# Optimization experiments

Hardware: AMD Instinct MI355X
Metric: run time of the kernel (lower is better)

Reference implementation:

```python
import jax, jax.numpy as jnp
import numpy as np

B, LI, LT = 1, 2048, 256
HID, HEADS, HD = 3072, 24, 128
MLP = 4 * HID  # 12288
EPS = 1e-6


def setup_inputs() -> dict:
    key = jax.random.key(0)
    ks = jax.random.split(key, 12)
    n = lambda k, s, sc=1.0: jax.random.normal(k, s, dtype=jnp.float32) * sc
    # RoPE tables, interleaved-pair layout over head_dim
    theta = 10000.0 ** (-jnp.arange(0, HD, 2, dtype=jnp.float32) / HD)  # [HD/2]
    ang = jnp.arange(LI, dtype=jnp.float32)[:, None] * theta[None, :]   # [LI, HD/2]
    freqs_cos = jnp.repeat(jnp.cos(ang), 2, axis=-1)  # [LI, HD]
    freqs_sin = jnp.repeat(jnp.sin(ang), 2, axis=-1)
    return {
        "img": n(ks[0], (B, LI, HID)),
        "txt": n(ks[1], (B, LT, HID)),
        "vec": n(ks[2], (B, HID)),
        "freqs_cos": freqs_cos,
        "freqs_sin": freqs_sin,
        "w1": n(ks[3], (3 * HID + MLP, HID), 0.02),
        "b1": jnp.zeros((3 * HID + MLP,), jnp.float32),
        "w2": n(ks[4], (HID, HID + MLP), 0.02),
        "b2": jnp.zeros((HID,), jnp.float32),
        "q_norm_w": jnp.ones((HD,), jnp.float32),
        "k_norm_w": jnp.ones((HD,), jnp.float32),
        "mod_w": n(ks[5], (3 * HID, HID), 0.02),
        "mod_b": jnp.zeros((3 * HID,), jnp.float32),
        "txt_len": LT,
    }


def _layernorm(x):  # no affine, eps=1e-6
    mu = x.mean(-1, keepdims=True)
    var = ((x - mu) ** 2).mean(-1, keepdims=True)
    return (x - mu) * jax.lax.rsqrt(var + EPS)


def _rmsnorm(x, w):  # per-head-dim RMSNorm with affine weight
    ms = (x * x).mean(-1, keepdims=True)
    return x * jax.lax.rsqrt(ms + EPS) * w


def _rope(x, cos, sin):  # x: [B,L,H,D]; interleaved complex rotation
    xr = x.reshape(*x.shape[:-1], HD // 2, 2)
    rot = jnp.stack([-xr[..., 1], xr[..., 0]], axis=-1).reshape(x.shape)
    return x * cos[None, :, None, :] + rot * sin[None, :, None, :]


def reference(img, txt, vec, freqs_cos, freqs_sin, w1, b1, w2, b2,
              q_norm_w, k_norm_w, mod_w, mod_b, txt_len):
    H = img.shape[-1]
    Li = img.shape[1]
    # modulation: SiLU(vec) @ W -> shift, scale, gate
    mod = jax.nn.silu(vec) @ mod_w.T + mod_b           # [B, 3H]
    shift, scale, gate = jnp.split(mod, 3, axis=-1)
    modulate = lambda x: x * (1.0 + scale[:, None, :]) + shift[:, None, :]
    img_mod = modulate(_layernorm(img))
    txt_mod = modulate(_layernorm(txt))
    x_mod = jnp.concatenate([img_mod, txt_mod], axis=1)  # [B,S,H]
    Bb, S = x_mod.shape[0], x_mod.shape[1]
    # fused QKV projection (slices of linear1)
    qkv = x_mod @ w1[: 3 * H].T + b1[: 3 * H]
    q, k, v = [t.reshape(Bb, S, HEADS, HD) for t in jnp.split(qkv, 3, axis=-1)]
    q = _rmsnorm(q, q_norm_w)
    k = _rmsnorm(k, k_norm_w)
    # RoPE only on the img portion of the sequence
    q = jnp.concatenate([_rope(q[:, :Li], freqs_cos, freqs_sin), q[:, Li:]], axis=1)
    k = jnp.concatenate([_rope(k[:, :Li], freqs_cos, freqs_sin), k[:, Li:]], axis=1)
    # full (non-causal) attention over img+txt tokens
    logits = jnp.einsum('bqhd,bkhd->bhqk', q, k) * (HD ** -0.5)
    probs = jax.nn.softmax(logits, axis=-1)
    attn = jnp.einsum('bhqk,bkhd->bqhd', probs, v).reshape(Bb, S, H)
    # MLP branch (linear1 mlp slice) with gelu-tanh, then fused linear2
    mlp = jax.nn.gelu(x_mod @ w1[3 * H:].T + b1[3 * H:], approximate=True)
    out = jnp.concatenate([attn, mlp], axis=-1) @ w2.T + b2  # [B,S,H]
    img_out = img + gate[:, None, :] * out[:, :-txt_len]
    txt_out = txt + gate[:, None, :] * out[:, -txt_len:]
    return img_out, txt_out
```

## Files before the change

### kernel.cpp

```cpp
#include <hip/hip_runtime.h>
#include <hip/hip_bf16.h>

#define DI __device__ __forceinline__

typedef __attribute__((ext_vector_type(8))) short bf8;
typedef __attribute__((ext_vector_type(4))) float f4;
typedef __attribute__((ext_vector_type(8))) unsigned short us8;

#define LI    2048
#define LT    256
#define SEQ   2304
#define HID   3072
#define NHEAD 24
#define HD    128
#define N1    21504
#define QKVW  9216
#define N2CAT 15360

DI unsigned short f2bf(float f) {
  union { float f; unsigned u; } v; v.f = f;
  unsigned r = v.u + 0x7FFFu + ((v.u >> 16) & 1u);
  return (unsigned short)(r >> 16);
}
DI float bf2f(unsigned short h) {
  union { unsigned u; float f; } v; v.u = ((unsigned)h) << 16;
  return v.f;
}

DI void gload16(const void* g, void* l) {
  __builtin_amdgcn_global_load_lds(
      (const __attribute__((address_space(1))) void*)g,
      (__attribute__((address_space(3))) void*)l, 16, 0, 0);
}

DI f4 mfma16(bf8 a, bf8 b, f4 c) {
  return __builtin_amdgcn_mfma_f32_16x16x32_bf16(a, b, c, 0, 0, 0);
}

__global__ void k_mod(const float* __restrict__ vec, const float* __restrict__ mw,
                      const float* __restrict__ mb, float* __restrict__ mod) {
  int row = blockIdx.x * 4 + (threadIdx.x >> 6);
  int lane = threadIdx.x & 63;
  const float4* wr = (const float4*)(mw + (size_t)row * HID);
  const float4* vv = (const float4*)vec;
  float s = 0.f;
  for (int i = lane; i < HID / 4; i += 64) {
    float4 w4 = wr[i], x4 = vv[i];
    s += (x4.x / (1.f + __expf(-x4.x))) * w4.x;
    s += (x4.y / (1.f + __expf(-x4.y))) * w4.y;
    s += (x4.z / (1.f + __expf(-x4.z))) * w4.z;
    s += (x4.w / (1.f + __expf(-x4.w))) * w4.w;
  }
#pragma unroll
  for (int m = 32; m; m >>= 1) s += __shfl_xor(s, m);
  if (lane == 0) mod[row] = s + mb[row];
}

__global__ void k_lnmod(const float* __restrict__ img, const float* __restrict__ txt,
                        const float* __restrict__ mod, unsigned short* __restrict__ xmod) {
  int t = blockIdx.x;
  const float* x = (t < LI) ? (img + (size_t)t * HID) : (txt + (size_t)(t - LI) * HID);
  const float4* x4 = (const float4*)x;
  float4 v[3];
  float s = 0.f, ss = 0.f;
#pragma unroll
  for (int j = 0; j < 3; ++j) {
    v[j] = x4[threadIdx.x + j * 256];
    s  += v[j].x + v[j].y + v[j].z + v[j].w;
    ss += v[j].x * v[j].x + v[j].y * v[j].y + v[j].z * v[j].z + v[j].w * v[j].w;
  }
#pragma unroll
  for (int m = 32; m; m >>= 1) { s += __shfl_xor(s, m); ss += __shfl_xor(ss, m); }
  __shared__ float red[8];
  int wv = threadIdx.x >> 6;
  if ((threadIdx.x & 63) == 0) { red[wv] = s; red[4 + wv] = ss; }
  __syncthreads();
  s = red[0] + red[1] + red[2] + red[3];
  ss = red[4] + red[5] + red[6] + red[7];
  float mu = s * (1.f / HID);
  float var = ss * (1.f / HID) - mu * mu;
  float inv = rsqrtf(var + 1e-6f);
  const float* shift = mod;
  const float* scale = mod + HID;
#pragma unroll
  for (int j = 0; j < 3; ++j) {
    int i = threadIdx.x + j * 256;
    int c = i * 4;
    ushort4 o;
    o.x = f2bf((v[j].x - mu) * inv * (1.f + scale[c + 0]) + shift[c + 0]);
    o.y = f2bf((v[j].y - mu) * inv * (1.f + scale[c + 1]) + shift[c + 1]);
    o.z = f2bf((v[j].z - mu) * inv * (1.f + scale[c + 2]) + shift[c + 2]);
    o.w = f2bf((v[j].w - mu) * inv * (1.f + scale[c + 3]) + shift[c + 3]);
    ((ushort4*)xmod)[(size_t)t * (HID / 4) + i] = o;
  }
}

__global__ void k_f2bf(const float* __restrict__ in, unsigned short* __restrict__ out, int n4) {
  int stride = gridDim.x * blockDim.x;
  for (int i = blockIdx.x * blockDim.x + threadIdx.x; i < n4; i += stride) {
    float4 f = ((const float4*)in)[i];
    ushort4 o;
    o.x = f2bf(f.x); o.y = f2bf(f.y); o.z = f2bf(f.z); o.w = f2bf(f.w);
    ((ushort4*)out)[i] = o;
  }
}

#define BAR()    asm volatile("s_barrier" ::: "memory")
#define VMCNT8() asm volatile("s_waitcnt vmcnt(8)" ::: "memory")
#define VMCNT6() asm volatile("s_waitcnt vmcnt(6)" ::: "memory")
#define VMCNT2() asm volatile("s_waitcnt vmcnt(2)" ::: "memory")
#define VMCNT0() asm volatile("s_waitcnt vmcnt(0)" ::: "memory")
#define LGKM0()  do { asm volatile("s_waitcnt lgkmcnt(0)" ::: "memory"); \
                      __builtin_amdgcn_sched_barrier(0); } while (0)

__global__ __launch_bounds__(512, 2) void k_gemm1(const unsigned short* __restrict__ xmod,
    const unsigned short* __restrict__ w1b, const float* __restrict__ b1,
    unsigned short* __restrict__ qkv, unsigned short* __restrict__ amlp) {
  __shared__ unsigned short As[2][256 * 64];
  __shared__ unsigned short Bs[2][256 * 64];
  const int K = HID;
  const int NT = K / 64;
  int tid = threadIdx.x, lane = tid & 63, wid = tid >> 6;
  int wr = wid >> 2, wc = wid & 3;

  int b = blockIdx.x;
  const int Q = 756 / 8, R = 756 % 8;
  int xcd = b & 7, idx = b >> 3;
  int wg = (xcd < R ? xcd * (Q + 1) : R * (Q + 1) + (xcd - R) * Q) + idx;
  int bm = wg % 9, bn = wg / 9;

  const unsigned short* Ag = xmod + (size_t)bm * 256 * K;
  const unsigned short* Bg = w1b + (size_t)bn * 256 * K;

  int sgran = (lane & 7) ^ ((lane >> 3) & 7);
  int srow = wid * 16 + (lane >> 3);

#define STAGE_A(bufi, t, hh) do { \
    gload16(Ag + (size_t)((hh)*128 + srow) * K + (t)*64 + sgran*8, \
            &As[bufi][((hh)*128 + wid*16) * 64]); \
    gload16(Ag + (size_t)((hh)*128 + 8 + srow) * K + (t)*64 + sgran*8, \
            &As[bufi][((hh)*128 + wid*16 + 8) * 64]); \
  } while (0)
#define STAGE_B(bufi, t, hh) do { \
    gload16(Bg + (size_t)((hh)*128 + srow) * K + (t)*64 + sgran*8, \
            &Bs[bufi][((hh)*128 + wid*16) * 64]); \
    gload16(Bg + (size_t)((hh)*128 + 8 + srow) * K + (t)*64 + sgran*8, \
            &Bs[bufi][((hh)*128 + wid*16 + 8) * 64]); \
  } while (0)

  int rA = wr * 128 + (lane & 15);
  int rB = wc * 64 + (lane & 15);
  int qq = lane >> 4, l7 = lane & 7;

  f4 acc[8][4];
#pragma unroll
  for (int m = 0; m < 8; ++m)
#pragma unroll
    for (int n = 0; n < 4; ++n) acc[m][n] = (f4){0.f, 0.f, 0.f, 0.f};
  bf8 aL[4][2], aH[4][2], bL[2][2], bH[2][2];

#define RD(buf, r, s) (*(const bf8*)&buf[(r) * 64 + ((((s)*4 + qq) ^ l7) << 3)])

#define GROUP(C, tn, tn2) do { \
    _Pragma("unroll") for (int m = 0; m < 4; ++m) \
      _Pragma("unroll") for (int s = 0; s < 2; ++s) aL[m][s] = RD(As[C], rA + m*16, s); \
    _Pragma("unroll") for (int n = 0; n < 2; ++n) \
      _Pragma("unroll") for (int s = 0; s < 2; ++s) bL[n][s] = RD(Bs[C], rB + n*16, s); \
    STAGE_A(1-(C), tn, 1); STAGE_B(1-(C), tn, 0); STAGE_B(1-(C), tn, 1); \
    LGKM0(); \
    __builtin_amdgcn_s_setprio(1); \
    _Pragma("unroll") for (int m = 0; m < 4; ++m) \
      _Pragma("unroll") for (int n = 0; n < 2; ++n) \
        _Pragma("unroll") for (int s = 0; s < 2; ++s) \
          acc[m][n] = mfma16(aL[m][s], bL[n][s], acc[m][n]); \
    __builtin_amdgcn_s_setprio(0); \
    _Pragma("unroll") for (int n = 0; n < 2; ++n) \
      _Pragma("unroll") for (int s = 0; s < 2; ++s) bH[n][s] = RD(Bs[C], rB + (n+2)*16, s); \
    LGKM0(); \
    __builtin_amdgcn_s_setprio(1); \
    _Pragma("unroll") for (int m = 0; m < 4; ++m) \
      _Pragma("unroll") for (int n = 0; n < 2; ++n) \
        _Pragma("unroll") for (int s = 0; s < 2; ++s) \
          acc[m][n+2] = mfma16(aL[m][s], bH[n][s], acc[m][n+2]); \
    __builtin_amdgcn_s_setprio(0); \
    _Pragma("unroll") for (int m = 0; m < 4; ++m) \
      _Pragma("unroll") for (int s = 0; s < 2; ++s) aH[m][s] = RD(As[C], rA + (m+4)*16, s); \
    LGKM0(); \
    BAR(); \
    __builtin_amdgcn_s_setprio(1); \
    _Pragma("unroll") for (int m = 0; m < 4; ++m) \
      _Pragma("unroll") for (int n = 0; n < 2; ++n) \
        _Pragma("unroll") for (int s = 0; s < 2; ++s) \
          acc[m+4][n+2] = mfma16(aH[m][s], bH[n][s], acc[m+4][n+2]); \
    __builtin_amdgcn_s_setprio(0); \
    STAGE_A(C, tn2, 0); \
    __builtin_amdgcn_s_setprio(1); \
    _Pragma("unroll") for (int m = 0; m < 4; ++m) \
      _Pragma("unroll") for (int n = 0; n < 2; ++n) \
        _Pragma("unroll") for (int s = 0; s < 2; ++s) \
          acc[m+4][n] = mfma16(aH[m][s], bL[n][s], acc[m+4][n]); \
    __builtin_amdgcn_s_setprio(0); \
    VMCNT2(); \
    BAR(); \
  } while (0)

  STAGE_A(0, 0, 0); STAGE_A(0, 0, 1); STAGE_B(0, 0, 0); STAGE_B(0, 0, 1);
  STAGE_A(1, 1, 0);
  VMCNT2();
  BAR();

  for (int i = 0; i < NT / 2; ++i) {
    int t0 = 2 * i;
    int n1 = t0 + 2; if (n1 > NT - 1) n1 = NT - 1;
    int n2 = t0 + 3; if (n2 > NT - 1) n2 = NT - 1;
    GROUP(0, t0 + 1, n1);
    GROUP(1, n1, n2);
  }
  VMCNT0();

  int r0 = bm * 256 + wr * 128 + ((lane >> 4) << 2);
  int c0 = bn * 256 + wc * 64 + (lane & 15);
  bool isqkv = (bn * 256) < QKVW;
#pragma unroll
  for (int m = 0; m < 8; ++m) {
#pragma unroll
    for (int n = 0; n < 4; ++n) {
      int col = c0 + n * 16;
      float bias = b1[col];
#pragma unroll
      for (int j = 0; j < 4; ++j) {
        int row = r0 + m * 16 + j;
        float v = acc[m][n][j] + bias;
        if (isqkv) {
          qkv[(size_t)row * QKVW + col] = f2bf(v);
        } else {
          float u = 0.7978845608f * (v + 0.044715f * v * v * v);
          float g = v / (1.f + __expf(-2.f * u));
          amlp[(size_t)row * N2CAT + (col - 6144)] = f2bf(g);
        }
      }
    }
  }
#undef STAGE_A
#undef STAGE_B
#undef RD
#undef GROUP
}

__global__ __launch_bounds__(512, 2) void k_gemm2(const unsigned short* __restrict__ amlp,
    const unsigned short* __restrict__ w2b, const float* __restrict__ b2,
    const float* __restrict__ img, const float* __restrict__ txt,
    const float* __restrict__ gate, float* __restrict__ out) {
  __shared__ unsigned short As[3][256 * 64];
  __shared__ unsigned short Bs[3][128 * 64];
  const int K = N2CAT;
  const int NT = K / 64;
  int tid = threadIdx.x, lane = tid & 63, wid = tid >> 6;
  int wr = wid >> 1, wc = wid & 1;

  int b = blockIdx.x;
  int bsw = (b & 7) * 27 + (b >> 3);
  int bm = bsw % 9, bn = bsw / 9;

  const unsigned short* Ag = amlp + (size_t)bm * 256 * K;
  const unsigned short* Bg = w2b + (size_t)bn * 128 * K;

  int sgran = (lane & 7) ^ ((lane >> 3) & 7);
  int srow = wid * 16 + (lane >> 3);

#define STAGE2_A(bufi, t, hh) do { \
    gload16(Ag + (size_t)((hh)*128 + srow) * K + (t)*64 + sgran*8, \
            &As[bufi][((hh)*128 + wid*16) * 64]); \
    gload16(Ag + (size_t)((hh)*128 + 8 + srow) * K + (t)*64 + sgran*8, \
            &As[bufi][((hh)*128 + wid*16 + 8) * 64]); \
  } while (0)
#define STAGE2_B(bufi, t) do { \
    gload16(Bg + (size_t)(srow) * K + (t)*64 + sgran*8, \
            &Bs[bufi][(wid*16) * 64]); \
    gload16(Bg + (size_t)(8 + srow) * K + (t)*64 + sgran*8, \
            &Bs[bufi][(wid*16 + 8) * 64]); \
  } while (0)

  int rA = wr * 64 + (lane & 15);
  int rB = wc * 64 + (lane & 15);
  int qq = lane >> 4, l7 = lane & 7;

  f4 acc[4][4];
#pragma unroll
  for (int m = 0; m < 4; ++m)
#pragma unroll
    for (int n = 0; n < 4; ++n) acc[m][n] = (f4){0.f, 0.f, 0.f, 0.f};
  bf8 aL[2][2], aH[2][2], bL[2][2], bH[2][2];

#define RD2(buf, r, s) (*(const bf8*)&buf[(r) * 64 + ((((s)*4 + qq) ^ l7) << 3)])

#define GROUP2(C, SB, t, full) do { \
    _Pragma("unroll") for (int m = 0; m < 2; ++m) \
      _Pragma("unroll") for (int s = 0; s < 2; ++s) aL[m][s] = RD2(As[C], rA + m*16, s); \
    _Pragma("unroll") for (int n = 0; n < 2; ++n) \
      _Pragma("unroll") for (int s = 0; s < 2; ++s) bL[n][s] = RD2(Bs[C], rB + n*16, s); \
    if (full) STAGE2_A(SB, (t) + 2, 0); \
    LGKM0(); \
    __builtin_amdgcn_s_setprio(1); \
    _Pragma("unroll") for (int m = 0; m < 2; ++m) \
      _Pragma("unroll") for (int n = 0; n < 2; ++n) \
        _Pragma("unroll") for (int s = 0; s < 2; ++s) \
          acc[m][n] = mfma16(aL[m][s], bL[n][s], acc[m][n]); \
    __builtin_amdgcn_s_setprio(0); \
    BAR(); \
    _Pragma("unroll") for (int n = 0; n < 2; ++n) \
      _Pragma("unroll") for (int s = 0; s < 2; ++s) bH[n][s] = RD2(Bs[C], rB + (n+2)*16, s); \
    if (full) STAGE2_A(SB, (t) + 2, 1); \
    LGKM0(); \
    __builtin_amdgcn_s_setprio(1); \
    _Pragma("unroll") for (int m = 0; m < 2; ++m) \
      _Pragma("unroll") for (int n = 0; n < 2; ++n) \
        _Pragma("unroll") for (int s = 0; s < 2; ++s) \
          acc[m][n+2] = mfma16(aL[m][s], bH[n][s], acc[m][n+2]); \
    __builtin_amdgcn_s_setprio(0); \
    BAR(); \
    _Pragma("unroll") for (int m = 0; m < 2; ++m) \
      _Pragma("unroll") for (int s = 0; s < 2; ++s) aH[m][s] = RD2(As[C], rA + (m+2)*16, s); \
    if (full) STAGE2_B(SB, (t) + 2); \
    LGKM0(); \
    __builtin_amdgcn_s_setprio(1); \
    _Pragma("unroll") for (int m = 0; m < 2; ++m) \
      _Pragma("unroll") for (int n = 0; n < 2; ++n) \
        _Pragma("unroll") for (int s = 0; s < 2; ++s) \
          acc[m+2][n+2] = mfma16(aH[m][s], bH[n][s], acc[m+2][n+2]); \
    __builtin_amdgcn_s_setprio(0); \
    BAR(); \
    __builtin_amdgcn_s_setprio(1); \
    _Pragma("unroll") for (int m = 0; m < 2; ++m) \
      _Pragma("unroll") for (int n = 0; n < 2; ++n) \
        _Pragma("unroll") for (int s = 0; s < 2; ++s) \
          acc[m+2][n] = mfma16(aH[m][s], bL[n][s], acc[m+2][n]); \
    __builtin_amdgcn_s_setprio(0); \
    if (full) { VMCNT6(); } else { VMCNT0(); } \
    BAR(); \
  } while (0)

  STAGE2_A(0, 0, 0); STAGE2_A(0, 0, 1); STAGE2_B(0, 0);
  STAGE2_A(1, 1, 0); STAGE2_A(1, 1, 1); STAGE2_B(1, 1);
  VMCNT6();
  BAR();

  for (int i = 0; i < NT / 3; ++i) {
    int t = 3 * i;
    GROUP2(0, 2, t,     (t + 2) < NT);
    GROUP2(1, 0, t + 1, (t + 3) < NT);
    GROUP2(2, 1, t + 2, (t + 4) < NT);
  }
  VMCNT0();

  int r0 = bm * 256 + wr * 64 + ((lane >> 4) << 2);
  int c0 = bn * 128 + wc * 64 + (lane & 15);
#pragma unroll
  for (int m = 0; m < 4; ++m) {
#pragma unroll
    for (int n = 0; n < 4; ++n) {
      int col = c0 + n * 16;
      float bias = b2[col];
      float gt = gate[col];
#pragma unroll
      for (int j = 0; j < 4; ++j) {
        int row = r0 + m * 16 + j;
        float v = acc[m][n][j] + bias;
        float res = (row < LI) ? img[(size_t)row * HID + col]
                               : txt[(size_t)(row - LI) * HID + col];
        out[(size_t)row * HID + col] = res + gt * v;
      }
    }
  }
#undef STAGE2_A
#undef STAGE2_B
#undef RD2
#undef GROUP2
}

__global__ void k_qkvt(unsigned short* __restrict__ qkv, const float* __restrict__ qw,
                       const float* __restrict__ kw, const float* __restrict__ fcos,
                       const float* __restrict__ fsin, unsigned short* __restrict__ vt) {
  int b = blockIdx.x;
  int tid = threadIdx.x;
  __shared__ unsigned short tile[64 * 65];
  if (b < 13824) {
    int gw = (b * 256 + tid) >> 6;
    int lane = tid & 63;
    int token = gw / NHEAD, head = gw - token * NHEAD;
    bool dorope = token < LI;
    float c = 1.f, sn = 0.f;
    if (dorope) { c = fcos[token * HD + 2 * lane]; sn = fsin[token * HD + 2 * lane]; }
#pragma unroll
    for (int qk = 0; qk < 2; ++qk) {
      unsigned short* p = qkv + (size_t)token * QKVW + qk * HID + head * HD;
      unsigned u = ((const unsigned*)p)[lane];
      float x0 = bf2f((unsigned short)(u & 0xffff));
      float x1 = bf2f((unsigned short)(u >> 16));
      float ss = x0 * x0 + x1 * x1;
#pragma unroll
      for (int m2 = 32; m2; m2 >>= 1) ss += __shfl_xor(ss, m2);
      float inv = rsqrtf(ss * (1.f / HD) + 1e-6f);
      const float* w = qk ? kw : qw;
      float y0 = x0 * inv * w[2 * lane];
      float y1 = x1 * inv * w[2 * lane + 1];
      if (dorope) { float r0 = y0 * c - y1 * sn; float r1 = y1 * c + y0 * sn; y0 = r0; y1 = r1; }
      ((unsigned*)p)[lane] = ((unsigned)f2bf(y0)) | (((unsigned)f2bf(y1)) << 16);
    }
  } else {
    int bb = b - 13824;
    int h = bb / 72; int rem = bb - h * 72; int tt = rem >> 1; int dd = rem & 1;
    int t0 = tt * 64, d0 = dd * 64;
#pragma unroll
    for (int j = 0; j < 2; ++j) {
      int idx = j * 256 + tid;
      int row = idx >> 3, s = idx & 7;
      us8 vv = *(const us8*)(qkv + (size_t)(t0 + row) * QKVW + 2 * HID + h * HD + d0 + s * 8);
#pragma unroll
      for (int i = 0; i < 8; ++i) tile[row * 65 + s * 8 + i] = vv[i];
    }
    __syncthreads();
#pragma unroll
    for (int j = 0; j < 2; ++j) {
      int idx = j * 256 + tid;
      int dr = idx >> 3, sl = idx & 7;
      us8 o;
#pragma unroll
      for (int i = 0; i < 8; ++i) o[i] = tile[(sl * 8 + i) * 65 + dr];
      *(us8*)(vt + (size_t)(h * HD + d0 + dr) * SEQ + t0 + sl * 8) = o;
    }
  }
}

__global__ __launch_bounds__(256) void k_attn(const unsigned short* __restrict__ qkv,
                                              const unsigned short* __restrict__ vt,
                                              unsigned short* __restrict__ amlp,
                                              const float* __restrict__ w2,
                                              unsigned short* __restrict__ w2b) {
  int b = blockIdx.x;
  int tid = threadIdx.x;
  if (b >= 864) {
    int cb = b - 864;
    const int n4 = HID * N2CAT / 4;
    for (int i = cb * 256 + tid; i < n4; i += 768 * 256) {
      float4 f = ((const float4*)w2)[i];
      ushort4 o;
      o.x = f2bf(f.x); o.y = f2bf(f.y); o.z = f2bf(f.z); o.w = f2bf(f.w);
      ((ushort4*)w2b)[i] = o;
    }
    return;
  }
  __shared__ unsigned short S[40960];
  unsigned short* Ks = S;
  unsigned short* Vs = S + 16384;
  unsigned short* Qs = S + 32768;
  unsigned short* Ps = S + 32768;

  int bsw = (b & 7) * 108 + (b >> 3);
  int head = bsw / 36, qt = bsw - head * 36;
  int lane = tid & 63, wv = tid >> 6;
  int qbase = qt * 64;

#define STAGEK(dst, t) do { \
    int rloc_ = tid >> 4, sl_ = tid & 15, slg_ = sl_ ^ (rloc_ & 7); \
    const unsigned short* kg_ = qkv + HID + (size_t)((t) * 64 + rloc_) * QKVW + head * HD + slg_ * 8; \
    _Pragma("unroll") for (int j = 0; j < 4; ++j) \
      gload16(kg_ + (size_t)(j * 16) * QKVW, &(dst)[(j * 256 + tid) * 8]); \
  } while (0)
#define STAGEV(dst, t) do { \
    int rloc_ = tid >> 3, sl_ = tid & 7, slg_ = sl_ ^ (rloc_ & 7); \
    const unsigned short* vg_ = vt + (size_t)(head * HD + rloc_) * SEQ + (t) * 64 + slg_ * 8; \
    _Pragma("unroll") for (int j = 0; j < 4; ++j) \
      gload16(vg_ + (size_t)(j * 32) * SEQ, &(dst)[(j * 256 + tid) * 8]); \
  } while (0)

  {
    int row = tid >> 4, sl = tid & 15;
    int slg = sl ^ (row & 7);
    const unsigned short* qg = qkv + (size_t)(qbase + row) * QKVW + head * HD + slg * 8;
#pragma unroll
    for (int j = 0; j < 4; ++j)
      gload16(qg + (size_t)(j * 16) * QKVW, &Qs[(j * 256 + tid) * 8]);
  }
  STAGEK(Ks, 0); STAGEV(Vs, 0);
  STAGEK(Ks + 8192, 1); STAGEV(Vs + 8192, 1);
  VMCNT8();
  BAR();

  bf8 qf[4];
#pragma unroll
  for (int kk = 0; kk < 4; ++kk) {
    int row = wv * 16 + (lane & 15);
    int col = (kk * 32 + ((lane >> 4) * 8)) ^ ((lane & 7) << 3);
    qf[kk] = *(const bf8*)&Qs[row * 128 + col];
  }
  LGKM0();
  BAR();

  float mrun[4], lrun[4];
  f4 oacc[8];
#pragma unroll
  for (int j = 0; j < 4; ++j) { mrun[j] = -1e30f; lrun[j] = 0.f; }
#pragma unroll
  for (int n = 0; n < 8; ++n) oacc[n] = (f4){0.f, 0.f, 0.f, 0.f};

  for (int kt = 0; kt < SEQ / 64; ++kt) {
    int cur = kt & 1;
    const unsigned short* Kc = Ks + cur * 8192;
    const unsigned short* Vc = Vs + cur * 8192;
    f4 sacc[4];
#pragma unroll
    for (int n = 0; n < 4; ++n) sacc[n] = (f4){0.f, 0.f, 0.f, 0.f};
#pragma unroll
    for (int kk = 0; kk < 4; ++kk) {
#pragma unroll
      for (int n = 0; n < 4; ++n) {
        int row = n * 16 + (lane & 15);
        int col = (kk * 32 + ((lane >> 4) * 8)) ^ ((lane & 7) << 3);
        bf8 kf = *(const bf8*)&Kc[row * 128 + col];
        sacc[n] = mfma16(qf[kk], kf, sacc[n]);
      }
    }
    const float SC = 0.08838834764831845f;
    float mj[4];
#pragma unroll
    for (int j = 0; j < 4; ++j)
      mj[j] = fmaxf(fmaxf(sacc[0][j], sacc[1][j]), fmaxf(sacc[2][j], sacc[3][j]));
#pragma unroll
    for (int j = 0; j < 4; ++j) {
#pragma unroll
      for (int mk = 8; mk; mk >>= 1) mj[j] = fmaxf(mj[j], __shfl_xor(mj[j], mk));
    }
    float resc[4], psum[4];
#pragma unroll
    for (int j = 0; j < 4; ++j) {
      float nm = fmaxf(mrun[j], mj[j] * SC);
      resc[j] = __expf(mrun[j] - nm);
      mrun[j] = nm;
      psum[j] = 0.f;
    }
#pragma unroll
    for (int n = 0; n < 4; ++n) {
#pragma unroll
      for (int j = 0; j < 4; ++j) {
        float p = __expf(sacc[n][j] * SC - mrun[j]);
        psum[j] += p;
        int row = wv * 16 + ((lane >> 4) << 2) + j;
        int col = (n * 16 + (lane & 15)) ^ ((row & 7) << 3);
        Ps[row * 64 + col] = f2bf(p);
      }
    }
#pragma unroll
    for (int j = 0; j < 4; ++j) {
#pragma unroll
      for (int mk = 8; mk; mk >>= 1) psum[j] += __shfl_xor(psum[j], mk);
      lrun[j] = lrun[j] * resc[j] + psum[j];
    }
#pragma unroll
    for (int n = 0; n < 8; ++n) {
#pragma unroll
      for (int j = 0; j < 4; ++j) oacc[n][j] *= resc[j];
    }
#pragma unroll
    for (int kk = 0; kk < 2; ++kk) {
      int prow = wv * 16 + (lane & 15);
      int pcol = (kk * 32 + ((lane >> 4) * 8)) ^ ((lane & 7) << 3);
      bf8 pa = *(const bf8*)&Ps[prow * 64 + pcol];
#pragma unroll
      for (int n = 0; n < 8; ++n) {
        int vrow = n * 16 + (lane & 15);
        int vcol = (kk * 32 + ((lane >> 4) * 8)) ^ ((vrow & 7) << 3);
        bf8 vf = *(const bf8*)&Vc[vrow * 64 + vcol];
        oacc[n] = mfma16(pa, vf, oacc[n]);
      }
    }
    BAR();
    if (kt + 2 < SEQ / 64) {
      STAGEK(Ks + cur * 8192, kt + 2);
      STAGEV(Vs + cur * 8192, kt + 2);
      VMCNT8();
    } else {
      VMCNT0();
    }
    BAR();
  }
#undef STAGEK
#undef STAGEV

#pragma unroll
  for (int j = 0; j < 4; ++j) {
    float invl = 1.f / lrun[j];
    int row = qbase + wv * 16 + ((lane >> 4) << 2) + j;
#pragma unroll
    for (int n = 0; n < 8; ++n) {
      int col = head * HD + n * 16 + (lane & 15);
      amlp[(size_t)row * N2CAT + col] = f2bf(oacc[n][j] * invl);
    }
  }
}

extern "C" void kernel_launch(void* const* d_in, const int* in_sizes, int n_in,
                              void* d_out, int out_size, void* d_ws, size_t ws_size,
                              hipStream_t stream) {
  (void)in_sizes; (void)n_in; (void)out_size; (void)ws_size;
  const float* img  = (const float*)d_in[0];
  const float* txt  = (const float*)d_in[1];
  const float* vec  = (const float*)d_in[2];
  const float* fcos = (const float*)d_in[3];
  const float* fsin = (const float*)d_in[4];
  const float* w1   = (const float*)d_in[5];
  const float* b1   = (const float*)d_in[6];
  const float* w2   = (const float*)d_in[7];
  const float* b2   = (const float*)d_in[8];
  const float* qnw  = (const float*)d_in[9];
  const float* knw  = (const float*)d_in[10];
  const float* mw   = (const float*)d_in[11];
  const float* mb   = (const float*)d_in[12];
  float* out = (float*)d_out;

  char* ws = (char*)d_ws;
  float*          mod  = (float*)(ws);
  unsigned short* xmod = (unsigned short*)(ws + 40960);
  unsigned short* w1b  = (unsigned short*)(ws + 14196736);
  unsigned short* qkv  = (unsigned short*)(ws + 146317312);
  unsigned short* amlp = (unsigned short*)(ws + 188784640);
  unsigned short* vtb  = xmod;
  unsigned short* w2b  = w1b;

  k_mod<<<QKVW / 4, 256, 0, stream>>>(vec, mw, mb, mod);
  k_lnmod<<<SEQ, 256, 0, stream>>>(img, txt, mod, xmod);
  k_f2bf<<<2048, 256, 0, stream>>>(w1, w1b, N1 * HID / 4);
  k_gemm1<<<756, 512, 0, stream>>>(xmod, w1b, b1, qkv, amlp);
  k_qkvt<<<13824 + 1728, 256, 0, stream>>>(qkv, qnw, knw, fcos, fsin, vtb);
  k_attn<<<864 + 768, 256, 0, stream>>>(qkv, vtb, amlp, w2, w2b);
  k_gemm2<<<216, 512, 0, stream>>>(amlp, w2b, b2, img, txt, mod + 2 * HID, out);
}
```

Baseline: 909.3 us.

## Fuse fp32-to-bf16 weight conversion into GEMM1 B-tile staging

Removes the standalone k_f2bf pass over w1 and has k_gemm1 load fp32 weight tiles directly into registers, convert them with packed bf16 conversion instructions, and write them to LDS, interleaved with the MFMA phases. This avoids a full read plus bf16 write of the 21504x3072 weight matrix before the GEMM. In exchange, GEMM1 now reads twice as many bytes for B (fp32, re-read by each of the 9 M-blocks), adds register pressure, and replaces async direct-to-LDS loads with register round trips, which may stall the pipeline.

```diff
diff --git a/kernel.cpp b/kernel.cpp
--- a/kernel.cpp
+++ b/kernel.cpp
@@ -95,16 +95,6 @@
   }
 }
 
-__global__ void k_f2bf(const float* __restrict__ in, unsigned short* __restrict__ out, int n4) {
-  int stride = gridDim.x * blockDim.x;
-  for (int i = blockIdx.x * blockDim.x + threadIdx.x; i < n4; i += stride) {
-    float4 f = ((const float4*)in)[i];
-    ushort4 o;
-    o.x = f2bf(f.x); o.y = f2bf(f.y); o.z = f2bf(f.z); o.w = f2bf(f.w);
-    ((ushort4*)out)[i] = o;
-  }
-}
-
 #define BAR()    asm volatile("s_barrier" ::: "memory")
 #define VMCNT8() asm volatile("s_waitcnt vmcnt(8)" ::: "memory")
 #define VMCNT6() asm volatile("s_waitcnt vmcnt(6)" ::: "memory")
@@ -114,7 +104,7 @@
                       __builtin_amdgcn_sched_barrier(0); } while (0)
 
 __global__ __launch_bounds__(512, 2) void k_gemm1(const unsigned short* __restrict__ xmod,
-    const unsigned short* __restrict__ w1b, const float* __restrict__ b1,
+    const float* __restrict__ w1f, const float* __restrict__ b1,
     unsigned short* __restrict__ qkv, unsigned short* __restrict__ amlp) {
   __shared__ unsigned short As[2][256 * 64];
   __shared__ unsigned short Bs[2][256 * 64];
@@ -130,7 +120,7 @@
   int bm = wg % 9, bn = wg / 9;
 
   const unsigned short* Ag = xmod + (size_t)bm * 256 * K;
-  const unsigned short* Bg = w1b + (size_t)bn * 256 * K;
+  const float* Bgf = w1f + (size_t)bn * 256 * K;
 
   int sgran = (lane & 7) ^ ((lane >> 3) & 7);
   int srow = wid * 16 + (lane >> 3);
@@ -141,11 +131,25 @@
     gload16(Ag + (size_t)((hh)*128 + 8 + srow) * K + (t)*64 + sgran*8, \
             &As[bufi][((hh)*128 + wid*16 + 8) * 64]); \
   } while (0)
-#define STAGE_B(bufi, t, hh) do { \
-    gload16(Bg + (size_t)((hh)*128 + srow) * K + (t)*64 + sgran*8, \
-            &Bs[bufi][((hh)*128 + wid*16) * 64]); \
-    gload16(Bg + (size_t)((hh)*128 + 8 + srow) * K + (t)*64 + sgran*8, \
-            &Bs[bufi][((hh)*128 + wid*16 + 8) * 64]); \
+
+#define BLOAD(t, hh, d) do { \
+    const float* s0_ = Bgf + (size_t)((hh)*128 + srow) * K + (t)*64 + sgran*8; \
+    const float* s1_ = s0_ + (size_t)8 * K; \
+    d[0] = *(const float4*)(s0_); d[1] = *(const float4*)(s0_ + 4); \
+    d[2] = *(const float4*)(s1_); d[3] = *(const float4*)(s1_ + 4); \
+  } while (0)
+#define BWRITE(bufi, hh, d) do { \
+    uint4 pk_; \
+    asm volatile("v_cvt_pk_bf16_f32 %0, %1, %2" : "=v"(pk_.x) : "v"(d[0].x), "v"(d[0].y)); \
+    asm volatile("v_cvt_pk_bf16_f32 %0, %1, %2" : "=v"(pk_.y) : "v"(d[0].z), "v"(d[0].w)); \
+    asm volatile("v_cvt_pk_bf16_f32 %0, %1, %2" : "=v"(pk_.z) : "v"(d[1].x), "v"(d[1].y)); \
+    asm volatile("v_cvt_pk_bf16_f32 %0, %1, %2" : "=v"(pk_.w) : "v"(d[1].z), "v"(d[1].w)); \
+    *(uint4*)&Bs[bufi][((hh)*128 + wid*16) * 64 + lane * 8] = pk_; \
+    asm volatile("v_cvt_pk_bf16_f32 %0, %1, %2" : "=v"(pk_.x) : "v"(d[2].x), "v"(d[2].y)); \
+    asm volatile("v_cvt_pk_bf16_f32 %0, %1, %2" : "=v"(pk_.y) : "v"(d[2].z), "v"(d[2].w)); \
+    asm volatile("v_cvt_pk_bf16_f32 %0, %1, %2" : "=v"(pk_.z) : "v"(d[3].x), "v"(d[3].y)); \
+    asm volatile("v_cvt_pk_bf16_f32 %0, %1, %2" : "=v"(pk_.w) : "v"(d[3].z), "v"(d[3].w)); \
+    *(uint4*)&Bs[bufi][((hh)*128 + wid*16 + 8) * 64 + lane * 8] = pk_; \
   } while (0)
 
   int rA = wr * 128 + (lane & 15);
@@ -162,11 +166,14 @@
 #define RD(buf, r, s) (*(const bf8*)&buf[(r) * 64 + ((((s)*4 + qq) ^ l7) << 3)])
 
 #define GROUP(C, tn, tn2) do { \
+    float4 bst[4]; \
+     \
     _Pragma("unroll") for (int m = 0; m < 4; ++m) \
       _Pragma("unroll") for (int s = 0; s < 2; ++s) aL[m][s] = RD(As[C], rA + m*16, s); \
     _Pragma("unroll") for (int n = 0; n < 2; ++n) \
       _Pragma("unroll") for (int s = 0; s < 2; ++s) bL[n][s] = RD(Bs[C], rB + n*16, s); \
-    STAGE_A(1-(C), tn, 1); STAGE_B(1-(C), tn, 0); STAGE_B(1-(C), tn, 1); \
+    BLOAD(tn, 0, bst); \
+    STAGE_A(1-(C), tn, 1); \
     LGKM0(); \
     __builtin_amdgcn_s_setprio(1); \
     _Pragma("unroll") for (int m = 0; m < 4; ++m) \
@@ -174,8 +181,11 @@
         _Pragma("unroll") for (int s = 0; s < 2; ++s) \
           acc[m][n] = mfma16(aL[m][s], bL[n][s], acc[m][n]); \
     __builtin_amdgcn_s_setprio(0); \
+     \
     _Pragma("unroll") for (int n = 0; n < 2; ++n) \
       _Pragma("unroll") for (int s = 0; s < 2; ++s) bH[n][s] = RD(Bs[C], rB + (n+2)*16, s); \
+    BWRITE(1-(C), 0, bst); \
+    BLOAD(tn, 1, bst); \
     LGKM0(); \
     __builtin_amdgcn_s_setprio(1); \
     _Pragma("unroll") for (int m = 0; m < 4; ++m) \
@@ -183,8 +193,10 @@
         _Pragma("unroll") for (int s = 0; s < 2; ++s) \
           acc[m][n+2] = mfma16(aL[m][s], bH[n][s], acc[m][n+2]); \
     __builtin_amdgcn_s_setprio(0); \
+     \
     _Pragma("unroll") for (int m = 0; m < 4; ++m) \
       _Pragma("unroll") for (int s = 0; s < 2; ++s) aH[m][s] = RD(As[C], rA + (m+4)*16, s); \
+    BWRITE(1-(C), 1, bst); \
     LGKM0(); \
     BAR(); \
     __builtin_amdgcn_s_setprio(1); \
@@ -193,6 +205,7 @@
         _Pragma("unroll") for (int s = 0; s < 2; ++s) \
           acc[m+4][n+2] = mfma16(aH[m][s], bH[n][s], acc[m+4][n+2]); \
     __builtin_amdgcn_s_setprio(0); \
+     \
     STAGE_A(C, tn2, 0); \
     __builtin_amdgcn_s_setprio(1); \
     _Pragma("unroll") for (int m = 0; m < 4; ++m) \
@@ -204,9 +217,15 @@
     BAR(); \
   } while (0)
 
-  STAGE_A(0, 0, 0); STAGE_A(0, 0, 1); STAGE_B(0, 0, 0); STAGE_B(0, 0, 1);
+  STAGE_A(0, 0, 0); STAGE_A(0, 0, 1);
+  {
+    float4 p0[4];
+    BLOAD(0, 0, p0); BWRITE(0, 0, p0);
+    BLOAD(0, 1, p0); BWRITE(0, 1, p0);
+  }
   STAGE_A(1, 1, 0);
   VMCNT2();
+  LGKM0();
   BAR();
 
   for (int i = 0; i < NT / 2; ++i) {
@@ -242,7 +261,8 @@
     }
   }
 #undef STAGE_A
-#undef STAGE_B
+#undef BLOAD
+#undef BWRITE
 #undef RD
 #undef GROUP
 }
@@ -621,16 +641,14 @@
   char* ws = (char*)d_ws;
   float*          mod  = (float*)(ws);
   unsigned short* xmod = (unsigned short*)(ws + 40960);
-  unsigned short* w1b  = (unsigned short*)(ws + 14196736);
+  unsigned short* w2b  = (unsigned short*)(ws + 14196736);
   unsigned short* qkv  = (unsigned short*)(ws + 146317312);
   unsigned short* amlp = (unsigned short*)(ws + 188784640);
   unsigned short* vtb  = xmod;
-  unsigned short* w2b  = w1b;
 
   k_mod<<<QKVW / 4, 256, 0, stream>>>(vec, mw, mb, mod);
   k_lnmod<<<SEQ, 256, 0, stream>>>(img, txt, mod, xmod);
-  k_f2bf<<<2048, 256, 0, stream>>>(w1, w1b, N1 * HID / 4);
-  k_gemm1<<<756, 512, 0, stream>>>(xmod, w1b, b1, qkv, amlp);
+  k_gemm1<<<756, 512, 0, stream>>>(xmod, w1, b1, qkv, amlp);
   k_qkvt<<<13824 + 1728, 256, 0, stream>>>(qkv, qnw, knw, fcos, fsin, vtb);
   k_attn<<<864 + 768, 256, 0, stream>>>(qkv, vtb, amlp, w2, w2b);
   k_gemm2<<<216, 512, 0, stream>>>(amlp, w2b, b2, img, txt, mod + 2 * HID, out);
```

New measurement: 944.4 us. +3.9%, slower.

## Fuse w1 bf16 cast into lnmod and enlarge attention query tile to 128

Applied to the files above, without the earlier changes.

The standalone w1 fp32-to-bf16 conversion kernel is folded into extra blocks of the layernorm/modulation kernel, which removes one launch and lets the cast overlap with the row normalization. The attention kernel moves to 512-thread blocks covering 128 query rows, so each K/V tile staged in shared memory serves twice as many queries and total K/V traffic is halved. Q fragments are now loaded straight from global memory into registers, skipping the shared-memory staging step, and the vmcnt waits are adjusted to match the smaller per-thread load count. Costs: fewer attention blocks (432), possible register and occupancy pressure under launch_bounds(512,4), and uncoalesced direct Q loads.

```diff
diff --git a/kernel.cpp b/kernel.cpp
--- a/kernel.cpp
+++ b/kernel.cpp
@@ -57,8 +57,20 @@
 }
 
 __global__ void k_lnmod(const float* __restrict__ img, const float* __restrict__ txt,
-                        const float* __restrict__ mod, unsigned short* __restrict__ xmod) {
+                        const float* __restrict__ mod, unsigned short* __restrict__ xmod,
+                        const float* __restrict__ w1, unsigned short* __restrict__ w1b) {
   int t = blockIdx.x;
+  if (t >= SEQ) {
+    int cb = t - SEQ;
+    const int n4 = N1 * HID / 4;
+    for (int i = cb * 256 + threadIdx.x; i < n4; i += 1024 * 256) {
+      float4 f = ((const float4*)w1)[i];
+      ushort4 o;
+      o.x = f2bf(f.x); o.y = f2bf(f.y); o.z = f2bf(f.z); o.w = f2bf(f.w);
+      ((ushort4*)w1b)[i] = o;
+    }
+    return;
+  }
   const float* x = (t < LI) ? (img + (size_t)t * HID) : (txt + (size_t)(t - LI) * HID);
   const float4* x4 = (const float4*)x;
   float4 v[3];
@@ -95,19 +107,10 @@
   }
 }
 
-__global__ void k_f2bf(const float* __restrict__ in, unsigned short* __restrict__ out, int n4) {
-  int stride = gridDim.x * blockDim.x;
-  for (int i = blockIdx.x * blockDim.x + threadIdx.x; i < n4; i += stride) {
-    float4 f = ((const float4*)in)[i];
-    ushort4 o;
-    o.x = f2bf(f.x); o.y = f2bf(f.y); o.z = f2bf(f.z); o.w = f2bf(f.w);
-    ((ushort4*)out)[i] = o;
-  }
-}
-
 #define BAR()    asm volatile("s_barrier" ::: "memory")
 #define VMCNT8() asm volatile("s_waitcnt vmcnt(8)" ::: "memory")
 #define VMCNT6() asm volatile("s_waitcnt vmcnt(6)" ::: "memory")
+#define VMCNT4() asm volatile("s_waitcnt vmcnt(4)" ::: "memory")
 #define VMCNT2() asm volatile("s_waitcnt vmcnt(2)" ::: "memory")
 #define VMCNT0() asm volatile("s_waitcnt vmcnt(0)" ::: "memory")
 #define LGKM0()  do { asm volatile("s_waitcnt lgkmcnt(0)" ::: "memory"); \
@@ -432,17 +435,17 @@
   }
 }
 
-__global__ __launch_bounds__(256) void k_attn(const unsigned short* __restrict__ qkv,
-                                              const unsigned short* __restrict__ vt,
-                                              unsigned short* __restrict__ amlp,
-                                              const float* __restrict__ w2,
-                                              unsigned short* __restrict__ w2b) {
+__global__ __launch_bounds__(512, 4) void k_attn(const unsigned short* __restrict__ qkv,
+                                                 const unsigned short* __restrict__ vt,
+                                                 unsigned short* __restrict__ amlp,
+                                                 const float* __restrict__ w2,
+                                                 unsigned short* __restrict__ w2b) {
   int b = blockIdx.x;
   int tid = threadIdx.x;
-  if (b >= 864) {
-    int cb = b - 864;
+  if (b >= 432) {
+    int cb = b - 432;
     const int n4 = HID * N2CAT / 4;
-    for (int i = cb * 256 + tid; i < n4; i += 768 * 256) {
+    for (int i = cb * 512 + tid; i < n4; i += 768 * 512) {
       float4 f = ((const float4*)w2)[i];
       ushort4 o;
       o.x = f2bf(f.x); o.y = f2bf(f.y); o.z = f2bf(f.z); o.w = f2bf(f.w);
@@ -453,48 +456,36 @@
   __shared__ unsigned short S[40960];
   unsigned short* Ks = S;
   unsigned short* Vs = S + 16384;
-  unsigned short* Qs = S + 32768;
   unsigned short* Ps = S + 32768;
 
-  int bsw = (b & 7) * 108 + (b >> 3);
-  int head = bsw / 36, qt = bsw - head * 36;
+  int bsw = (b & 7) * 54 + (b >> 3);
+  int head = bsw / 18, qt = bsw - head * 18;
   int lane = tid & 63, wv = tid >> 6;
-  int qbase = qt * 64;
+  int qbase = qt * 128;
 
 #define STAGEK(dst, t) do { \
-    int rloc_ = tid >> 4, sl_ = tid & 15, slg_ = sl_ ^ (rloc_ & 7); \
-    const unsigned short* kg_ = qkv + HID + (size_t)((t) * 64 + rloc_) * QKVW + head * HD + slg_ * 8; \
-    _Pragma("unroll") for (int j = 0; j < 4; ++j) \
-      gload16(kg_ + (size_t)(j * 16) * QKVW, &(dst)[(j * 256 + tid) * 8]); \
+    int rl_ = tid >> 4, sl_ = tid & 15, sg_ = sl_ ^ (rl_ & 7); \
+    const unsigned short* kg_ = qkv + HID + (size_t)((t) * 64 + rl_) * QKVW + head * HD + sg_ * 8; \
+    gload16(kg_, &(dst)[tid * 8]); \
+    gload16(kg_ + (size_t)32 * QKVW, &(dst)[(512 + tid) * 8]); \
   } while (0)
 #define STAGEV(dst, t) do { \
-    int rloc_ = tid >> 3, sl_ = tid & 7, slg_ = sl_ ^ (rloc_ & 7); \
-    const unsigned short* vg_ = vt + (size_t)(head * HD + rloc_) * SEQ + (t) * 64 + slg_ * 8; \
-    _Pragma("unroll") for (int j = 0; j < 4; ++j) \
-      gload16(vg_ + (size_t)(j * 32) * SEQ, &(dst)[(j * 256 + tid) * 8]); \
-  } while (0)
-
+    int rl_ = tid >> 3, sl_ = tid & 7, sg_ = sl_ ^ (rl_ & 7); \
+    const unsigned short* vg_ = vt + (size_t)(head * HD + rl_) * SEQ + (t) * 64 + sg_ * 8; \
+    gload16(vg_, &(dst)[tid * 8]); \
+    gload16(vg_ + (size_t)64 * SEQ, &(dst)[(512 + tid) * 8]); \
+  } while (0)
+
+  bf8 qf[4];
   {
-    int row = tid >> 4, sl = tid & 15;
-    int slg = sl ^ (row & 7);
-    const unsigned short* qg = qkv + (size_t)(qbase + row) * QKVW + head * HD + slg * 8;
-#pragma unroll
-    for (int j = 0; j < 4; ++j)
-      gload16(qg + (size_t)(j * 16) * QKVW, &Qs[(j * 256 + tid) * 8]);
+    const unsigned short* qp =
+        qkv + (size_t)(qbase + wv * 16 + (lane & 15)) * QKVW + head * HD + (lane >> 4) * 8;
+#pragma unroll
+    for (int kk = 0; kk < 4; ++kk) qf[kk] = *(const bf8*)(qp + kk * 32);
   }
   STAGEK(Ks, 0); STAGEV(Vs, 0);
   STAGEK(Ks + 8192, 1); STAGEV(Vs + 8192, 1);
-  VMCNT8();
-  BAR();
-
-  bf8 qf[4];
-#pragma unroll
-  for (int kk = 0; kk < 4; ++kk) {
-    int row = wv * 16 + (lane & 15);
-    int col = (kk * 32 + ((lane >> 4) * 8)) ^ ((lane & 7) << 3);
-    qf[kk] = *(const bf8*)&Qs[row * 128 + col];
-  }
-  LGKM0();
+  VMCNT4();
   BAR();
 
   float mrun[4], lrun[4];
@@ -578,7 +569,7 @@
     if (kt + 2 < SEQ / 64) {
       STAGEK(Ks + cur * 8192, kt + 2);
       STAGEV(Vs + cur * 8192, kt + 2);
-      VMCNT8();
+      VMCNT4();
     } else {
       VMCNT0();
     }
@@ -628,10 +619,9 @@
   unsigned short* w2b  = w1b;
 
   k_mod<<<QKVW / 4, 256, 0, stream>>>(vec, mw, mb, mod);
-  k_lnmod<<<SEQ, 256, 0, stream>>>(img, txt, mod, xmod);
-  k_f2bf<<<2048, 256, 0, stream>>>(w1, w1b, N1 * HID / 4);
+  k_lnmod<<<SEQ + 1024, 256, 0, stream>>>(img, txt, mod, xmod, w1, w1b);
   k_gemm1<<<756, 512, 0, stream>>>(xmod, w1b, b1, qkv, amlp);
   k_qkvt<<<13824 + 1728, 256, 0, stream>>>(qkv, qnw, knw, fcos, fsin, vtb);
-  k_attn<<<864 + 768, 256, 0, stream>>>(qkv, vtb, amlp, w2, w2b);
+  k_attn<<<432 + 768, 512, 0, stream>>>(qkv, vtb, amlp, w2, w2b);
   k_gemm2<<<216, 512, 0, stream>>>(amlp, w2b, b2, img, txt, mod + 2 * HID, out);
 }
```

After: 875.6 us. -3.7%, faster.
